# Kernel tuning notes

Hardware: AMD Instinct MI355X
Metric: run time of the kernel (lower is better)

## Reference

```python
import jax, jax.numpy as jnp
import numpy as np

LN_EPS = 1e-5

def setup_inputs() -> dict:
    key = jax.random.key(0)
    ks = jax.random.split(key, 6)
    B, H, W, C = 32, 128, 96, 128
    ch = C // 2
    x = jax.random.normal(ks[0], (B, H, W, C), dtype=jnp.float32)
    # he_normal-style scaled init for 1x1 conv kernels (fan_in = C or ch)
    wq_ch = jax.random.normal(ks[1], (C,), dtype=jnp.float32) * np.float32(np.sqrt(2.0 / C))
    wv_ch = jax.random.normal(ks[2], (C, ch), dtype=jnp.float32) * np.float32(np.sqrt(2.0 / C))
    w_ch = jax.random.normal(ks[3], (ch, C), dtype=jnp.float32) * np.float32(np.sqrt(2.0 / ch))
    gamma = jnp.ones((C,), dtype=jnp.float32)
    beta = jnp.zeros((C,), dtype=jnp.float32)
    wq_sp = jax.random.normal(ks[4], (C, ch), dtype=jnp.float32) * np.float32(np.sqrt(2.0 / C))
    wv_sp = jax.random.normal(ks[5], (C, ch), dtype=jnp.float32) * np.float32(np.sqrt(2.0 / C))
    return {"x": x, "wq_ch": wq_ch, "wv_ch": wv_ch, "w_ch": w_ch,
            "gamma": gamma, "beta": beta, "wq_sp": wq_sp, "wv_sp": wv_sp}


def reference(x, wq_ch, wv_ch, w_ch, gamma, beta, wq_sp, wv_sp):
    B, H, W, C = x.shape
    hw = H * W
    ch = C // 2

    # ---- channel-only self-attention ----
    # q: 1x1 conv C->1, flatten to [B, HW], softmax over spatial positions
    q = jnp.einsum('bhwc,c->bhw', x, wq_ch).reshape(B, hw)
    q = jax.nn.softmax(q, axis=-1)
    # v: 1x1 conv C->C/2, flatten to [B, HW, C/2]
    v = jnp.einsum('bhwc,cd->bhwd', x, wv_ch).reshape(B, hw, ch)
    ctx = jnp.einsum('bn,bnd->bd', q, v)          # [B, C/2]
    ctx = ctx @ w_ch                               # 1x1 conv C/2 -> C, [B, C]
    # LayerNorm over axes [1,2,3] of (B,1,1,C) == per-sample norm over C
    mu = jnp.mean(ctx, axis=-1, keepdims=True)
    var = jnp.mean(jnp.square(ctx - mu), axis=-1, keepdims=True)
    ctx = (ctx - mu) * jax.lax.rsqrt(var + LN_EPS) * gamma + beta
    mask_ch = jax.nn.sigmoid(ctx)                  # [B, C]
    ch_out = x * mask_ch[:, None, None, :]

    # ---- spatial-only self-attention (parallel mode: input is x) ----
    # 1x1 conv C->C/2 followed by global avg pool == avg-pooled x projected
    q_sp = jnp.einsum('bhwc,cd->bd', x, wq_sp) / hw  # [B, C/2]
    q_sp = jax.nn.softmax(q_sp, axis=-1)
    v_sp = jnp.einsum('bhwc,cd->bhwd', x, wv_sp).reshape(B, hw, ch)
    sp_ctx = jnp.einsum('bd,bnd->bn', q_sp, v_sp).reshape(B, H, W, 1)
    sp_out = x * jax.nn.sigmoid(sp_ctx)

    return ch_out + sp_out
```

## Files before the change

kernel.cpp:

```cpp
#include <hip/hip_runtime.h>

#define BSZ 32
#define CC  128
#define CH  64
#define HWN 12288
#define BPB 64
#define ROWS_PER_BLOCK (HWN / BPB)

using f4 = __attribute__((ext_vector_type(4))) float;

__global__ __launch_bounds__(256) void psa_pass1(
    const float* __restrict__ x, const float* __restrict__ wq_ch,
    float* __restrict__ pS, float* __restrict__ pX, float* __restrict__ pZ)
{
    const int b    = blockIdx.x / BPB;
    const int blk  = blockIdx.x % BPB;
    const int tid  = threadIdx.x;
    const int l32  = tid & 31;
    const int slot = tid >> 5;

    const f4 wq = reinterpret_cast<const f4*>(wq_ch)[l32];

    float s0=0.f,s1=0.f,s2=0.f,s3=0.f;
    float a0=0.f,a1=0.f,a2=0.f,a3=0.f;
    float zacc=0.f;

    const float* xb = x + (size_t)b * (size_t)(HWN * CC);
    const int row0 = blk * ROWS_PER_BLOCK;

    for (int i = slot; i < ROWS_PER_BLOCK; i += 8) {
        const f4 xv = reinterpret_cast<const f4*>(xb + (size_t)(row0 + i) * CC)[l32];
        float p = xv.x*wq.x + xv.y*wq.y + xv.z*wq.z + xv.w*wq.w;
        p += __shfl_xor(p, 1);  p += __shfl_xor(p, 2);  p += __shfl_xor(p, 4);
        p += __shfl_xor(p, 8);  p += __shfl_xor(p, 16);
        const float e = __expf(p);
        if (l32 == 0) zacc += e;
        s0 += e*xv.x; s1 += e*xv.y; s2 += e*xv.z; s3 += e*xv.w;
        a0 += xv.x;   a1 += xv.y;   a2 += xv.z;   a3 += xv.w;
    }

    __shared__ float Ssh[CC];
    __shared__ float Xsh[CC];
    __shared__ float zsh;
    if (tid < CC) { Ssh[tid] = 0.f; Xsh[tid] = 0.f; }
    if (tid == 0) zsh = 0.f;
    __syncthreads();

    const int cb = l32 * 4;
    atomicAdd(&Ssh[cb+0], s0); atomicAdd(&Ssh[cb+1], s1);
    atomicAdd(&Ssh[cb+2], s2); atomicAdd(&Ssh[cb+3], s3);
    atomicAdd(&Xsh[cb+0], a0); atomicAdd(&Xsh[cb+1], a1);
    atomicAdd(&Xsh[cb+2], a2); atomicAdd(&Xsh[cb+3], a3);
    if (l32 == 0) atomicAdd(&zsh, zacc);
    __syncthreads();

    const size_t base = (size_t)(b * BPB + blk) * CC;
    if (tid < CC) {
        pS[base + tid] = Ssh[tid];
        pX[base + tid] = Xsh[tid];
    }
    if (tid == 0) pZ[b * BPB + blk] = zsh;
}

__global__ __launch_bounds__(128) void psa_mid(
    const float* __restrict__ pS, const float* __restrict__ pX,
    const float* __restrict__ pZ,
    const float* __restrict__ wv_ch, const float* __restrict__ w_ch,
    const float* __restrict__ gamma, const float* __restrict__ beta,
    const float* __restrict__ wq_sp, const float* __restrict__ wv_sp,
    float* __restrict__ mask_ch, float* __restrict__ wf)
{
    const int b = blockIdx.x;
    const int t = threadIdx.x;

    __shared__ float Ssh[CC], Xsh[CC], ctxh[CH], qsp[CH], zsh, red2[2];

    {
        const float* pSb = pS + (size_t)b * BPB * CC;
        const float* pXb = pX + (size_t)b * BPB * CC;
        float s = 0.f, a = 0.f;
        #pragma unroll
        for (int k = 0; k < BPB; ++k) {
            s += pSb[(size_t)k * CC + t];
            a += pXb[(size_t)k * CC + t];
        }
        Ssh[t] = s; Xsh[t] = a;
    }
    if (t < 64) {
        float z = pZ[b * BPB + t];
        z += __shfl_xor(z, 1); z += __shfl_xor(z, 2);  z += __shfl_xor(z, 4);
        z += __shfl_xor(z, 8); z += __shfl_xor(z, 16); z += __shfl_xor(z, 32);
        if (t == 0) zsh = z;
    }
    __syncthreads();

    if (t < CH) {
        float a = 0.f, aq = 0.f;
        #pragma unroll
        for (int c = 0; c < CC; ++c) {
            a  += Ssh[c] * wv_ch[c*CH + t];
            aq += Xsh[c] * wq_sp[c*CH + t];
        }
        ctxh[t] = a / zsh;
        float q = aq * (1.0f / (float)HWN);
        float m = q;
        m = fmaxf(m, __shfl_xor(m, 1));  m = fmaxf(m, __shfl_xor(m, 2));
        m = fmaxf(m, __shfl_xor(m, 4));  m = fmaxf(m, __shfl_xor(m, 8));
        m = fmaxf(m, __shfl_xor(m, 16)); m = fmaxf(m, __shfl_xor(m, 32));
        float e = __expf(q - m);
        float sum = e;
        sum += __shfl_xor(sum, 1);  sum += __shfl_xor(sum, 2);
        sum += __shfl_xor(sum, 4);  sum += __shfl_xor(sum, 8);
        sum += __shfl_xor(sum, 16); sum += __shfl_xor(sum, 32);
        qsp[t] = e / sum;
    }
    __syncthreads();

    float ctx = 0.f;
    #pragma unroll
    for (int d = 0; d < CH; ++d) ctx += ctxh[d] * w_ch[d*CC + t];

    const int wid = t >> 6;
    {
        float r = ctx;
        r += __shfl_xor(r, 1);  r += __shfl_xor(r, 2);  r += __shfl_xor(r, 4);
        r += __shfl_xor(r, 8);  r += __shfl_xor(r, 16); r += __shfl_xor(r, 32);
        if ((t & 63) == 0) red2[wid] = r;
    }
    __syncthreads();
    const float mu = (red2[0] + red2[1]) * (1.0f / CC);
    __syncthreads();
    const float dc = ctx - mu;
    {
        float r = dc * dc;
        r += __shfl_xor(r, 1);  r += __shfl_xor(r, 2);  r += __shfl_xor(r, 4);
        r += __shfl_xor(r, 8);  r += __shfl_xor(r, 16); r += __shfl_xor(r, 32);
        if ((t & 63) == 0) red2[wid] = r;
    }
    __syncthreads();
    const float var = (red2[0] + red2[1]) * (1.0f / CC);

    const float nrm = dc * rsqrtf(var + 1e-5f) * gamma[t] + beta[t];
    mask_ch[b*CC + t] = 1.0f / (1.0f + __expf(-nrm));

    float wacc = 0.f;
    #pragma unroll
    for (int d = 0; d < CH; ++d) wacc += wv_sp[t*CH + d] * qsp[d];
    wf[b*CC + t] = wacc;
}

__global__ __launch_bounds__(256) void psa_pass2(
    const float* __restrict__ x, const float* __restrict__ mask_ch,
    const float* __restrict__ wf, float* __restrict__ out)
{
    const int b    = blockIdx.x / BPB;
    const int blk  = blockIdx.x % BPB;
    const int tid  = threadIdx.x;
    const int l32  = tid & 31;
    const int slot = tid >> 5;

    const f4 m4 = reinterpret_cast<const f4*>(mask_ch + b*CC)[l32];
    const f4 w4 = reinterpret_cast<const f4*>(wf + b*CC)[l32];

    const float* xb = x   + (size_t)b * (size_t)(HWN * CC);
    float*       ob = out + (size_t)b * (size_t)(HWN * CC);
    const int row0 = blk * ROWS_PER_BLOCK;

    for (int i = slot; i < ROWS_PER_BLOCK; i += 8) {
        const size_t off = (size_t)(row0 + i) * CC;
        const f4 xv = reinterpret_cast<const f4*>(xb + off)[l32];
        float p = xv.x*w4.x + xv.y*w4.y + xv.z*w4.z + xv.w*w4.w;
        p += __shfl_xor(p, 1);  p += __shfl_xor(p, 2);  p += __shfl_xor(p, 4);
        p += __shfl_xor(p, 8);  p += __shfl_xor(p, 16);
        const float g = 1.0f / (1.0f + __expf(-p));
        f4 o;
        o.x = xv.x * (m4.x + g);
        o.y = xv.y * (m4.y + g);
        o.z = xv.z * (m4.z + g);
        o.w = xv.w * (m4.w + g);
        __builtin_nontemporal_store(o, reinterpret_cast<f4*>(ob + off) + l32);
    }
}

extern "C" void kernel_launch(void* const* d_in, const int* in_sizes, int n_in,
                              void* d_out, int out_size, void* d_ws, size_t ws_size,
                              hipStream_t stream) {
    const float* x     = (const float*)d_in[0];
    const float* wq_ch = (const float*)d_in[1];
    const float* wv_ch = (const float*)d_in[2];
    const float* w_ch  = (const float*)d_in[3];
    const float* gamma = (const float*)d_in[4];
    const float* beta  = (const float*)d_in[5];
    const float* wq_sp = (const float*)d_in[6];
    const float* wv_sp = (const float*)d_in[7];
    float* out = (float*)d_out;

    float* ws   = (float*)d_ws;
    float* pS   = ws;
    float* pX   = pS + (size_t)BSZ*BPB*CC;
    float* pZ   = pX + (size_t)BSZ*BPB*CC;
    float* mask = pZ + BSZ*BPB;
    float* wf   = mask + BSZ*CC;

    psa_pass1<<<BSZ*BPB, 256, 0, stream>>>(x, wq_ch, pS, pX, pZ);
    psa_mid  <<<BSZ,     128, 0, stream>>>(pS, pX, pZ, wv_ch, w_ch, gamma, beta,
                                           wq_sp, wv_sp, mask, wf);
    psa_pass2<<<BSZ*BPB, 256, 0, stream>>>(x, mask, wf, out);
}
```

Baseline: 126.6 us.

## Fuse three passes into one persistent kernel with per-batch spin barrier

Merges the reduction pass, the per-batch mid computation and the output pass into a single kernel. Blocks of the same batch synchronize through a global atomic counter with spin-wait, so each block computes the mid-stage itself and then re-reads its slice of x, hopefully while it is still cached. Blocks per batch halve to 1024 total so all can be co-resident with launch_bounds(256,4), and loops are unrolled by two. The second pass runs over rows in reverse order to hit recently loaded lines. This removes two kernel launches and the mask/wf round trip. The cost is redundant mid-stage work in every block and a deadlock risk if the blocks are not all resident at once.

```diff
diff --git a/kernel.cpp b/kernel.cpp
--- a/kernel.cpp
+++ b/kernel.cpp
@@ -4,44 +4,60 @@
 #define CC  128
 #define CH  64
 #define HWN 12288
-#define BPB 64
-#define ROWS_PER_BLOCK (HWN / BPB)
+#define BPB 32
+#define NBLK (BSZ*BPB)
+#define ROWS (HWN/BPB)
 
 using f4 = __attribute__((ext_vector_type(4))) float;
 
-__global__ __launch_bounds__(256) void psa_pass1(
+__global__ __launch_bounds__(256, 4) void psa_fused(
     const float* __restrict__ x, const float* __restrict__ wq_ch,
-    float* __restrict__ pS, float* __restrict__ pX, float* __restrict__ pZ)
+    const float* __restrict__ wv_ch, const float* __restrict__ w_ch,
+    const float* __restrict__ gamma, const float* __restrict__ beta,
+    const float* __restrict__ wq_sp, const float* __restrict__ wv_sp,
+    float* __restrict__ out,
+    float* __restrict__ pS, float* __restrict__ pX, float* __restrict__ pZ,
+    unsigned* __restrict__ counters)
 {
-    const int b    = blockIdx.x / BPB;
-    const int blk  = blockIdx.x % BPB;
+    const int b    = blockIdx.x & 31;
+    const int blk  = blockIdx.x >> 5;
     const int tid  = threadIdx.x;
     const int l32  = tid & 31;
     const int slot = tid >> 5;
 
+    __shared__ __align__(16) float Ssh[CC], Xsh[CC];
+    __shared__ __align__(16) float ctxh[CH], qsp[CH];
+    __shared__ __align__(16) float mask_sh[CC], wf_sh[CC];
+    __shared__ float zsh, red2[2];
+
+    const float* xb  = x + (size_t)b * (size_t)(HWN * CC);
+    const int   row0 = blk * ROWS;
+
     const f4 wq = reinterpret_cast<const f4*>(wq_ch)[l32];
 
     float s0=0.f,s1=0.f,s2=0.f,s3=0.f;
     float a0=0.f,a1=0.f,a2=0.f,a3=0.f;
     float zacc=0.f;
 
-    const float* xb = x + (size_t)b * (size_t)(HWN * CC);
-    const int row0 = blk * ROWS_PER_BLOCK;
-
-    for (int i = slot; i < ROWS_PER_BLOCK; i += 8) {
-        const f4 xv = reinterpret_cast<const f4*>(xb + (size_t)(row0 + i) * CC)[l32];
-        float p = xv.x*wq.x + xv.y*wq.y + xv.z*wq.z + xv.w*wq.w;
-        p += __shfl_xor(p, 1);  p += __shfl_xor(p, 2);  p += __shfl_xor(p, 4);
-        p += __shfl_xor(p, 8);  p += __shfl_xor(p, 16);
-        const float e = __expf(p);
-        if (l32 == 0) zacc += e;
-        s0 += e*xv.x; s1 += e*xv.y; s2 += e*xv.z; s3 += e*xv.w;
-        a0 += xv.x;   a1 += xv.y;   a2 += xv.z;   a3 += xv.w;
-    }
-
-    __shared__ float Ssh[CC];
-    __shared__ float Xsh[CC];
-    __shared__ float zsh;
+    for (int i = slot; i < ROWS; i += 16) {
+        const f4 xA = reinterpret_cast<const f4*>(xb + (size_t)(row0 + i)     * CC)[l32];
+        const f4 xB = reinterpret_cast<const f4*>(xb + (size_t)(row0 + i + 8) * CC)[l32];
+        float pA = xA.x*wq.x + xA.y*wq.y + xA.z*wq.z + xA.w*wq.w;
+        float pB = xB.x*wq.x + xB.y*wq.y + xB.z*wq.z + xB.w*wq.w;
+        pA += __shfl_xor(pA, 1);  pB += __shfl_xor(pB, 1);
+        pA += __shfl_xor(pA, 2);  pB += __shfl_xor(pB, 2);
+        pA += __shfl_xor(pA, 4);  pB += __shfl_xor(pB, 4);
+        pA += __shfl_xor(pA, 8);  pB += __shfl_xor(pB, 8);
+        pA += __shfl_xor(pA, 16); pB += __shfl_xor(pB, 16);
+        const float eA = __expf(pA);
+        const float eB = __expf(pB);
+        if (l32 == 0) zacc += eA + eB;
+        s0 += eA*xA.x + eB*xB.x;  s1 += eA*xA.y + eB*xB.y;
+        s2 += eA*xA.z + eB*xB.z;  s3 += eA*xA.w + eB*xB.w;
+        a0 += xA.x + xB.x;  a1 += xA.y + xB.y;
+        a2 += xA.z + xB.z;  a3 += xA.w + xB.w;
+    }
+
     if (tid < CC) { Ssh[tid] = 0.f; Xsh[tid] = 0.f; }
     if (tid == 0) zsh = 0.f;
     __syncthreads();
@@ -54,54 +70,53 @@
     if (l32 == 0) atomicAdd(&zsh, zacc);
     __syncthreads();
 
-    const size_t base = (size_t)(b * BPB + blk) * CC;
+    const size_t pbase = (size_t)(b * BPB + blk) * CC;
     if (tid < CC) {
-        pS[base + tid] = Ssh[tid];
-        pX[base + tid] = Xsh[tid];
+        pS[pbase + tid] = Ssh[tid];
+        pX[pbase + tid] = Xsh[tid];
     }
     if (tid == 0) pZ[b * BPB + blk] = zsh;
-}
-
-__global__ __launch_bounds__(128) void psa_mid(
-    const float* __restrict__ pS, const float* __restrict__ pX,
-    const float* __restrict__ pZ,
-    const float* __restrict__ wv_ch, const float* __restrict__ w_ch,
-    const float* __restrict__ gamma, const float* __restrict__ beta,
-    const float* __restrict__ wq_sp, const float* __restrict__ wv_sp,
-    float* __restrict__ mask_ch, float* __restrict__ wf)
-{
-    const int b = blockIdx.x;
-    const int t = threadIdx.x;
-
-    __shared__ float Ssh[CC], Xsh[CC], ctxh[CH], qsp[CH], zsh, red2[2];
+
+    __syncthreads();
+    __threadfence();
+    if (tid == 0) {
+        atomicAdd(&counters[b], 1u);
+        while (__hip_atomic_load(&counters[b], __ATOMIC_RELAXED,
+                                 __HIP_MEMORY_SCOPE_AGENT) < (unsigned)BPB)
+            __builtin_amdgcn_s_sleep(8);
+    }
+    __syncthreads();
+    __threadfence();
 
     {
         const float* pSb = pS + (size_t)b * BPB * CC;
         const float* pXb = pX + (size_t)b * BPB * CC;
-        float s = 0.f, a = 0.f;
-        #pragma unroll
-        for (int k = 0; k < BPB; ++k) {
-            s += pSb[(size_t)k * CC + t];
-            a += pXb[(size_t)k * CC + t];
+        if (tid < CC) {
+            float s = 0.f, a = 0.f;
+            #pragma unroll
+            for (int k = 0; k < BPB; ++k) {
+                s += pSb[(size_t)k * CC + tid];
+                a += pXb[(size_t)k * CC + tid];
+            }
+            Ssh[tid] = s; Xsh[tid] = a;
         }
-        Ssh[t] = s; Xsh[t] = a;
-    }
-    if (t < 64) {
-        float z = pZ[b * BPB + t];
-        z += __shfl_xor(z, 1); z += __shfl_xor(z, 2);  z += __shfl_xor(z, 4);
-        z += __shfl_xor(z, 8); z += __shfl_xor(z, 16); z += __shfl_xor(z, 32);
-        if (t == 0) zsh = z;
-    }
-    __syncthreads();
-
-    if (t < CH) {
+        if (tid < 32) {
+            float z = pZ[b * BPB + tid];
+            z += __shfl_xor(z, 1); z += __shfl_xor(z, 2); z += __shfl_xor(z, 4);
+            z += __shfl_xor(z, 8); z += __shfl_xor(z, 16);
+            if (tid == 0) zsh = z;
+        }
+    }
+    __syncthreads();
+
+    if (tid < CH) {
         float a = 0.f, aq = 0.f;
         #pragma unroll
         for (int c = 0; c < CC; ++c) {
-            a  += Ssh[c] * wv_ch[c*CH + t];
-            aq += Xsh[c] * wq_sp[c*CH + t];
+            a  += Ssh[c] * wv_ch[c*CH + tid];
+            aq += Xsh[c] * wq_sp[c*CH + tid];
         }
-        ctxh[t] = a / zsh;
+        ctxh[tid] = a / zsh;
         float q = aq * (1.0f / (float)HWN);
         float m = q;
         m = fmaxf(m, __shfl_xor(m, 1));  m = fmaxf(m, __shfl_xor(m, 2));
@@ -112,73 +127,69 @@
         sum += __shfl_xor(sum, 1);  sum += __shfl_xor(sum, 2);
         sum += __shfl_xor(sum, 4);  sum += __shfl_xor(sum, 8);
         sum += __shfl_xor(sum, 16); sum += __shfl_xor(sum, 32);
-        qsp[t] = e / sum;
+        qsp[tid] = e / sum;
     }
     __syncthreads();
 
     float ctx = 0.f;
-    #pragma unroll
-    for (int d = 0; d < CH; ++d) ctx += ctxh[d] * w_ch[d*CC + t];
-
-    const int wid = t >> 6;
+    if (tid < CC) {
+        #pragma unroll
+        for (int d = 0; d < CH; ++d) ctx += ctxh[d] * w_ch[d*CC + tid];
+    }
     {
-        float r = ctx;
+        float r = (tid < CC) ? ctx : 0.f;
         r += __shfl_xor(r, 1);  r += __shfl_xor(r, 2);  r += __shfl_xor(r, 4);
         r += __shfl_xor(r, 8);  r += __shfl_xor(r, 16); r += __shfl_xor(r, 32);
-        if ((t & 63) == 0) red2[wid] = r;
+        if ((tid & 63) == 0 && tid < CC) red2[tid >> 6] = r;
     }
     __syncthreads();
     const float mu = (red2[0] + red2[1]) * (1.0f / CC);
     __syncthreads();
-    const float dc = ctx - mu;
+    const float dc = (tid < CC) ? (ctx - mu) : 0.f;
     {
         float r = dc * dc;
         r += __shfl_xor(r, 1);  r += __shfl_xor(r, 2);  r += __shfl_xor(r, 4);
         r += __shfl_xor(r, 8);  r += __shfl_xor(r, 16); r += __shfl_xor(r, 32);
-        if ((t & 63) == 0) red2[wid] = r;
+        if ((tid & 63) == 0 && tid < CC) red2[tid >> 6] = r;
     }
     __syncthreads();
     const float var = (red2[0] + red2[1]) * (1.0f / CC);
 
-    const float nrm = dc * rsqrtf(var + 1e-5f) * gamma[t] + beta[t];
-    mask_ch[b*CC + t] = 1.0f / (1.0f + __expf(-nrm));
-
-    float wacc = 0.f;
-    #pragma unroll
-    for (int d = 0; d < CH; ++d) wacc += wv_sp[t*CH + d] * qsp[d];
-    wf[b*CC + t] = wacc;
-}
-
-__global__ __launch_bounds__(256) void psa_pass2(
-    const float* __restrict__ x, const float* __restrict__ mask_ch,
-    const float* __restrict__ wf, float* __restrict__ out)
-{
-    const int b    = blockIdx.x / BPB;
-    const int blk  = blockIdx.x % BPB;
-    const int tid  = threadIdx.x;
-    const int l32  = tid & 31;
-    const int slot = tid >> 5;
-
-    const f4 m4 = reinterpret_cast<const f4*>(mask_ch + b*CC)[l32];
-    const f4 w4 = reinterpret_cast<const f4*>(wf + b*CC)[l32];
-
-    const float* xb = x   + (size_t)b * (size_t)(HWN * CC);
-    float*       ob = out + (size_t)b * (size_t)(HWN * CC);
-    const int row0 = blk * ROWS_PER_BLOCK;
-
-    for (int i = slot; i < ROWS_PER_BLOCK; i += 8) {
-        const size_t off = (size_t)(row0 + i) * CC;
-        const f4 xv = reinterpret_cast<const f4*>(xb + off)[l32];
-        float p = xv.x*w4.x + xv.y*w4.y + xv.z*w4.z + xv.w*w4.w;
-        p += __shfl_xor(p, 1);  p += __shfl_xor(p, 2);  p += __shfl_xor(p, 4);
-        p += __shfl_xor(p, 8);  p += __shfl_xor(p, 16);
-        const float g = 1.0f / (1.0f + __expf(-p));
-        f4 o;
-        o.x = xv.x * (m4.x + g);
-        o.y = xv.y * (m4.y + g);
-        o.z = xv.z * (m4.z + g);
-        o.w = xv.w * (m4.w + g);
-        __builtin_nontemporal_store(o, reinterpret_cast<f4*>(ob + off) + l32);
+    if (tid < CC) {
+        const float nrm = dc * rsqrtf(var + 1e-5f) * gamma[tid] + beta[tid];
+        mask_sh[tid] = 1.0f / (1.0f + __expf(-nrm));
+        float wacc = 0.f;
+        #pragma unroll
+        for (int d = 0; d < CH; ++d) wacc += wv_sp[tid*CH + d] * qsp[d];
+        wf_sh[tid] = wacc;
+    }
+    __syncthreads();
+
+    const f4 m4 = reinterpret_cast<const f4*>(mask_sh)[l32];
+    const f4 w4 = reinterpret_cast<const f4*>(wf_sh)[l32];
+    float* ob = out + (size_t)b * (size_t)(HWN * CC);
+
+    for (int i = ROWS - 16 + slot; i >= 0; i -= 16) {
+        const size_t offA = (size_t)(row0 + i)     * CC;
+        const size_t offB = (size_t)(row0 + i + 8) * CC;
+        const f4 xA = reinterpret_cast<const f4*>(xb + offA)[l32];
+        const f4 xB = reinterpret_cast<const f4*>(xb + offB)[l32];
+        float pA = xA.x*w4.x + xA.y*w4.y + xA.z*w4.z + xA.w*w4.w;
+        float pB = xB.x*w4.x + xB.y*w4.y + xB.z*w4.z + xB.w*w4.w;
+        pA += __shfl_xor(pA, 1);  pB += __shfl_xor(pB, 1);
+        pA += __shfl_xor(pA, 2);  pB += __shfl_xor(pB, 2);
+        pA += __shfl_xor(pA, 4);  pB += __shfl_xor(pB, 4);
+        pA += __shfl_xor(pA, 8);  pB += __shfl_xor(pB, 8);
+        pA += __shfl_xor(pA, 16); pB += __shfl_xor(pB, 16);
+        const float gA = 1.0f / (1.0f + __expf(-pA));
+        const float gB = 1.0f / (1.0f + __expf(-pB));
+        f4 oA, oB;
+        oA.x = xA.x * (m4.x + gA); oA.y = xA.y * (m4.y + gA);
+        oA.z = xA.z * (m4.z + gA); oA.w = xA.w * (m4.w + gA);
+        oB.x = xB.x * (m4.x + gB); oB.y = xB.y * (m4.y + gB);
+        oB.z = xB.z * (m4.z + gB); oB.w = xB.w * (m4.w + gB);
+        __builtin_nontemporal_store(oA, reinterpret_cast<f4*>(ob + offA) + l32);
+        __builtin_nontemporal_store(oB, reinterpret_cast<f4*>(ob + offB) + l32);
     }
 }
 
@@ -195,15 +206,14 @@
     const float* wv_sp = (const float*)d_in[7];
     float* out = (float*)d_out;
 
-    float* ws   = (float*)d_ws;
-    float* pS   = ws;
-    float* pX   = pS + (size_t)BSZ*BPB*CC;
-    float* pZ   = pX + (size_t)BSZ*BPB*CC;
-    float* mask = pZ + BSZ*BPB;
-    float* wf   = mask + BSZ*CC;
-
-    psa_pass1<<<BSZ*BPB, 256, 0, stream>>>(x, wq_ch, pS, pX, pZ);
-    psa_mid  <<<BSZ,     128, 0, stream>>>(pS, pX, pZ, wv_ch, w_ch, gamma, beta,
-                                           wq_sp, wv_sp, mask, wf);
-    psa_pass2<<<BSZ*BPB, 256, 0, stream>>>(x, mask, wf, out);
+    float* ws = (float*)d_ws;
+    float* pS = ws;
+    float* pX = pS + (size_t)BSZ*BPB*CC;
+    float* pZ = pX + (size_t)BSZ*BPB*CC;
+    unsigned* counters = (unsigned*)(pZ + BSZ*BPB);
+
+    hipMemsetAsync((void*)counters, 0, BSZ * sizeof(unsigned), stream);
+
+    psa_fused<<<NBLK, 256, 0, stream>>>(x, wq_ch, wv_ch, w_ch, gamma, beta,
+                                        wq_sp, wv_sp, out, pS, pX, pZ, counters);
 }
```

Result: slower. 272.1 us (+114.9%).
